# Optimization experiments

Measured on AMD Instinct MI355X. Metric: run time of the kernel, lower is better.

Reference implementation:

```python
import jax, jax.numpy as jnp
import numpy as np
import math

G = 8; N0 = 16384; DEG = 8; E = G * N0 * DEG
C = 128; H = 256; OUT = 128; L = 3
RATIO = 0.5; EPS_FA = 0.1


def setup_inputs():
    key = jax.random.key(0)
    ks = jax.random.split(key, 10)
    x = jax.random.normal(ks[0], (G * N0, C), jnp.float32)
    e = jax.random.randint(ks[1], (2, E), 0, N0)
    off = jnp.repeat(jnp.arange(G) * N0, N0 * DEG)  # per-graph node offsets
    edge_index = (e + off[None, :]).astype(jnp.int32)  # (2, E), edges stay within their graph
    batch = jnp.repeat(jnp.arange(G), N0).astype(jnp.int32)
    root = jax.random.normal(ks[2], (G, C), jnp.float32)
    s = 0.05
    att_l = jax.random.normal(ks[3], (L, C), jnp.float32) * s
    att_r = jax.random.normal(ks[4], (L, C), jnp.float32) * s
    w_ih = jax.random.normal(ks[5], (3 * H, C * L), jnp.float32) * s
    w_hh = jax.random.normal(ks[6], (3 * H, H), jnp.float32) * s
    b_ih = jnp.zeros(3 * H, jnp.float32)
    b_hh = jnp.zeros(3 * H, jnp.float32)
    w_fin = jax.random.normal(ks[7], (OUT, H), jnp.float32) * s
    b_fin = jnp.zeros(OUT, jnp.float32)
    w_root = jax.random.normal(ks[8], (OUT, C), jnp.float32) * s
    b_root = jnp.zeros(OUT, jnp.float32)
    residual_alpha = jnp.float32(0.5)
    return dict(x=x, edge_index=edge_index, batch=batch, root=root, att_l=att_l, att_r=att_r,
                w_ih=w_ih, w_hh=w_hh, b_ih=b_ih, b_hh=b_hh, w_fin=w_fin, b_fin=b_fin,
                w_root=w_root, b_root=b_root, residual_alpha=residual_alpha)


def _faconv(xc, x0, src, dst, emask, al_w, ar_w, n):
    # gcn_norm with self-loops: deg over dst (+1 for self loop), w_ij = d_i^-1/2 d_j^-1/2
    deg = jax.ops.segment_sum(emask, dst, num_segments=n) + 1.0
    dinv = jax.lax.rsqrt(deg)
    w = dinv[src] * dinv[dst] * emask
    al = xc @ al_w  # (n,)
    ar = xc @ ar_w
    alpha = jnp.tanh(al[dst] + ar[src])
    out = jax.ops.segment_sum((w * alpha)[:, None] * xc[src], dst, num_segments=n)
    # self-loop message (weight 1/deg_i, alpha = tanh(al_i + ar_i))
    out = out + ((dinv * dinv) * jnp.tanh(al + ar))[:, None] * xc
    return out + EPS_FA * x0


def _forward(x, root, att_l, att_r, w_ih, w_hh, b_ih, b_hh, w_fin, b_fin, w_root, b_root, residual_alpha, edge_index):
    src = edge_index[0]
    dst = edge_index[1]
    emask = jnp.ones(src.shape[0], jnp.float32)  # edge validity mask (replaces dynamic edge filtering)
    cur, orig = x, x
    npg = N0  # nodes per graph at current layer (static)
    outs = []
    for i in range(L):
        n = G * npg
        h = jax.nn.relu(_faconv(cur, orig, src, dst, emask, att_l[i], att_r[i], n))
        outs.append(h.reshape(G, npg, C).max(axis=1))  # global_max_pool per graph
        # ASTGPool: score = out-degree on edge_index[0], per-graph top-k (k = ceil(npg*ratio))
        score = jax.ops.segment_sum(emask, src, num_segments=n)
        k = int(math.ceil(npg * RATIO))
        _, idx = jax.lax.top_k(score.reshape(G, npg), k)
        perm = (idx + (jnp.arange(G) * npg)[:, None]).reshape(-1)  # (G*k,) global kept-node ids
        keep = jnp.zeros(n, bool).at[perm].set(True)
        emask = emask * keep[src].astype(jnp.float32) * keep[dst].astype(jnp.float32)
        nmap = jnp.zeros(n, src.dtype).at[perm].set(jnp.arange(G * k, dtype=src.dtype))
        src, dst = nmap[src], nmap[dst]  # dead edges map to node 0 but have emask==0
        cur, orig, npg = h[perm], orig[perm], k  # multiplier = 1.0
    fused = jnp.concatenate(outs, axis=1)  # (G, C*L)
    # single-step GRU with h0 = 0
    gi = fused @ w_ih.T + b_ih
    ir, iz, inn = jnp.split(gi, 3, axis=1)
    br, bz, bn = jnp.split(b_hh, 3)
    r = jax.nn.sigmoid(ir + br)
    z = jax.nn.sigmoid(iz + bz)
    ncand = jnp.tanh(inn + r * bn)
    hgru = (1.0 - z) * ncand
    gnn_emb = hgru @ w_fin.T + b_fin
    root_emb = root @ w_root.T + b_root
    return residual_alpha * gnn_emb + (1.0 - residual_alpha) * root_emb


def reference(x, edge_index, batch, root, att_l, att_r, w_ih, w_hh, b_ih, b_hh, w_fin, b_fin, w_root, b_root, residual_alpha):
    del batch  # graphs are contiguous equal-size blocks; batch structure is encoded in G, N0
    return _forward(x, root, att_l, att_r, w_ih, w_hh, b_ih, b_hh, w_fin, b_fin, w_root, b_root, residual_alpha, edge_index)
```

## Files before the change

kernel.cpp:

```cpp
#include <hip/hip_runtime.h>
#include <math.h>

#define G 8
#define N0 16384
#define NEDGE (G*N0*8)
#define EPG (NEDGE/G)
#define C 128
#define EPS_FA 0.1f
#define SMAX 2048

typedef unsigned short ushort_t;
typedef unsigned int uint_t;

__device__ inline ushort_t f2bf(float f) {
    uint_t u = __float_as_uint(f);
    uint_t r = (u + 0x7FFFu + ((u >> 16) & 1u)) >> 16;
    return (ushort_t)r;
}
__device__ inline uint_t pack2bf(float a, float b) {
    return (uint_t)f2bf(a) | ((uint_t)f2bf(b) << 16);
}
__device__ inline float bflo(uint_t w) { return __uint_as_float(w << 16); }
__device__ inline float bfhi(uint_t w) { return __uint_as_float(w & 0xFFFF0000u); }

__global__ void __launch_bounds__(256) k_hist0(const int* __restrict__ ei,
                                               unsigned int* __restrict__ bh,
                                               ushort_t* __restrict__ lrank) {
    __shared__ unsigned int h[N0];
    int t = threadIdx.x;
    for (int i = t; i < N0; i += 256) h[i] = 0;
    __syncthreads();
    int base = blockIdx.x * 8192;
    int gbase = (blockIdx.x >> 4) * N0;
    for (int i = t; i < 8192; i += 256) {
        int s = ei[base + i] - gbase;
        int d = ei[NEDGE + base + i] - gbase;
        unsigned int old = atomicAdd(&h[d], 1u);
        lrank[base + i] = (ushort_t)(old & 0xFFFFu);
        atomicAdd(&h[s], 0x10000u);
    }
    __syncthreads();
    unsigned int* o = bh + (size_t)blockIdx.x * N0;
    for (int i = t; i < N0; i += 256) o[i] = h[i];
}

__global__ void __launch_bounds__(256) k_sumdeg_alar(
        unsigned int* __restrict__ bh, int* __restrict__ degI, int* __restrict__ score,
        float* __restrict__ pooled,
        const float* __restrict__ x, const float* __restrict__ attl,
        const float* __restrict__ attr, float* __restrict__ al, float* __restrict__ ar,
        ushort_t* __restrict__ xb) {
    int t = threadIdx.x;
    if ((int)blockIdx.x < 512) {
        int i = blockIdx.x * 256 + t;
        if (i < G * 384) pooled[i] = 0.0f;
        unsigned int* p = bh + ((size_t)((i >> 14) * 16) << 14) + (i & 16383);
        unsigned int run = 0; int as = 0;
        for (int b = 0; b < 16; b++) {
            unsigned int w = p[(size_t)b << 14];
            p[(size_t)b << 14] = run;
            run += w & 0xFFFFu; as += (int)(w >> 16);
        }
        degI[i] = (int)run; score[i] = as;
    } else {
        int idx = (blockIdx.x - 512) * 256 + t;
        int wid = idx >> 6, lane = idx & 63;
        float2 v  = ((const float2*)(x + (size_t)wid * C))[lane];
        ((uint_t*)(xb + (size_t)wid * C))[lane] = pack2bf(v.x, v.y);
        float2 l2 = ((const float2*)attl)[lane];
        float2 r2 = ((const float2*)attr)[lane];
        float sl = v.x * l2.x + v.y * l2.y;
        float sr = v.x * r2.x + v.y * r2.y;
        for (int o = 32; o >= 1; o >>= 1) { sl += __shfl_xor(sl, o); sr += __shfl_xor(sr, o); }
        if (lane == 0) { al[wid] = sl; ar[wid] = sr; }
    }
}

__global__ void k_sumdeg(unsigned int* __restrict__ bh, int* __restrict__ degI,
                         int* __restrict__ score, int shift, int nsub, int n) {
    int i = blockIdx.x * 256 + threadIdx.x;
    if (i >= n) return;
    int bins = 1 << shift;
    int g = i >> shift, u = i & (bins - 1);
    unsigned int* p = bh + ((size_t)(g * nsub) << shift) + u;
    unsigned int run = 0; int as = 0;
    for (int b = 0; b < nsub; b++) {
        unsigned int w = p[(size_t)b * bins];
        p[(size_t)b * bins] = run;
        run += w & 0xFFFFu; as += (int)(w >> 16);
    }
    degI[i] = (int)run; score[i] = as;
}

__global__ void __launch_bounds__(256) k_scan1(const int* __restrict__ degI,
                                               int* __restrict__ rowptr,
                                               int* __restrict__ bsum) {
    __shared__ int part[256];
    int t = threadIdx.x;
    int base = blockIdx.x * 2048 + t * 8;
    int v[8]; int s = 0;
    for (int i = 0; i < 8; i++) { v[i] = degI[base + i]; s += v[i]; }
    part[t] = s; __syncthreads();
    for (int o = 1; o < 256; o <<= 1) {
        int val = part[t];
        int add = (t >= o) ? part[t - o] : 0;
        __syncthreads();
        part[t] = val + add;
        __syncthreads();
    }
    int run = (t == 0) ? 0 : part[t - 1];
    if (t == 255) bsum[blockIdx.x] = part[255];
    for (int i = 0; i < 8; i++) { rowptr[base + i] = run; run += v[i]; }
}

__global__ void k_scan3s(int* __restrict__ rowptr,
                         const int* __restrict__ bsum, const int* __restrict__ degI,
                         const float* __restrict__ al, const float* __restrict__ ar,
                         float* __restrict__ dinv, float* __restrict__ selfco,
                         unsigned char* __restrict__ keep, int* __restrict__ nmap, int n) {
    __shared__ int base_s;
    int t = threadIdx.x;
    if (t < 64) {
        int c = blockIdx.x >> 3;
        int vv = (t < c) ? bsum[t] : 0;
        for (int o = 32; o >= 1; o >>= 1) vv += __shfl_xor(vv, o);
        if (t == 0) base_s = vv;
    }
    __syncthreads();
    int i = blockIdx.x * 256 + t;
    if (i >= n) return;
    rowptr[i] += base_s;
    float d  = (float)degI[i] + 1.0f;
    float di = rsqrtf(d);
    dinv[i]   = di;
    selfco[i] = di * di * tanhf(al[i] + ar[i]);
    keep[i] = 0; nmap[i] = 0;
}

__global__ void __launch_bounds__(256) k_fill_hist(
        const int* __restrict__ src, const int* __restrict__ dst,
        const unsigned char* __restrict__ em,
        const float* __restrict__ dinv, const float* __restrict__ al,
        const float* __restrict__ ar,
        const int* __restrict__ rowptr, const unsigned int* __restrict__ bpre,
        const ushort_t* __restrict__ lrank, int2* __restrict__ edges,
        int ebShift, int nsubShift, int binShift,
        const int* __restrict__ score, int npg, int nb,
        int* __restrict__ blockhist, int histBlocks) {
    __shared__ int lh[SMAX];
    int t = threadIdx.x;
    if ((int)blockIdx.x < histBlocks) {
        int g = blockIdx.x / nb, b = blockIdx.x % nb;
        for (int s = t; s < SMAX; s += 256) lh[s] = 0;
        __syncthreads();
        int s = score[g * npg + b * 256 + t];
        if (s > SMAX - 1) s = SMAX - 1;
        atomicAdd(&lh[s], 1);
        __syncthreads();
        int* outp = blockhist + ((size_t)g * nb + b) * SMAX;
        for (int i = t; i < SMAX; i += 256) outp[i] = lh[i];
    } else {
        int fb = blockIdx.x - histBlocks;
        int gph = fb & 7, chunk = fb >> 3;
        int e = gph * EPG + chunk * 256 + t;
        if (em && !em[e]) return;
        int s = src[e], d = dst[e];
        float cf = dinv[s] * dinv[d] * tanhf(al[d] + ar[s]);
        int b = e >> ebShift;
        int gb = (b >> nsubShift) << binShift;
        int slot = rowptr[d] + (int)bpre[((size_t)b << binShift) + (d - gb)] + (int)lrank[e];
        edges[slot] = make_int2(s, __float_as_int(cf));
    }
}

#define ACC4(W, CF) { a0 += (CF) * bflo((W).x); a1 += (CF) * bfhi((W).x); \
                      a2 += (CF) * bflo((W).y); a3 += (CF) * bfhi((W).y); }
__global__ void __launch_bounds__(256) k_msg_bp(
        const int* __restrict__ rowptr, const int* __restrict__ degI,
        const int2* __restrict__ edges,
        const ushort_t* __restrict__ cur, const ushort_t* __restrict__ xb,
        const int* __restrict__ oidx, const float* __restrict__ selfco,
        ushort_t* __restrict__ h, float* __restrict__ pb, int npg,
        int* __restrict__ blockhist, int* __restrict__ histT, int nb, int bpBlocks) {
    __shared__ float pm[8 * 128];
    __shared__ int tile[4096];
    int t = threadIdx.x;
    if ((int)blockIdx.x < bpBlocks) {
        int g = blockIdx.x >> 5, ch = blockIdx.x & 31;
        int s0 = ch * 64;
        int* bg = blockhist + (size_t)g * nb * SMAX;
        int tot = nb * 64;
        for (int i = t; i < tot; i += 256)
            tile[i] = bg[(size_t)(i >> 6) * SMAX + s0 + (i & 63)];
        __syncthreads();
        if (t < 64) {
            int acc = 0;
            for (int b = 0; b < nb; b++) {
                int idx = b * 64 + t;
                int v = tile[idx]; tile[idx] = acc; acc += v;
            }
            histT[g * SMAX + s0 + t] = acc;
        }
        __syncthreads();
        for (int i = t; i < tot; i += 256)
            bg[(size_t)(i >> 6) * SMAX + s0 + (i & 63)] = tile[i];
        return;
    }
    int mb   = blockIdx.x - bpBlocks;
    int g    = mb & 7;
    int ib   = mb >> 3;
    int sub  = t >> 5;
    int lane = t & 31;
    int v = g * npg + ib * 8 + sub;
    int rs = rowptr[v], deg = degI[v];
    int o = oidx ? oidx[v] : v;
    uint2 cw = ((const uint2*)(cur + (size_t)v * C))[lane];
    uint2 xw = ((const uint2*)(xb  + (size_t)o * C))[lane];
    float sc = selfco[v];
    float a0 = 0.0f, a1 = 0.0f, a2 = 0.0f, a3 = 0.0f;
    for (int j0 = 0; j0 < deg; j0 += 32) {
        int cnt = deg - j0; if (cnt > 32) cnt = 32;
        int2 er = make_int2(0, 0);
        if (lane < cnt) er = edges[rs + j0 + lane];
        uint2 w0 = make_uint2(0,0), w1 = w0, w2 = w0, w3 = w0;
        {
            int s0 = __shfl(er.x, 0, 32);
            if (0 < cnt) w0 = ((const uint2*)(cur + (size_t)s0 * C))[lane];
            int s1 = __shfl(er.x, 1, 32);
            if (1 < cnt) w1 = ((const uint2*)(cur + (size_t)s1 * C))[lane];
            int s2 = __shfl(er.x, 2, 32);
            if (2 < cnt) w2 = ((const uint2*)(cur + (size_t)s2 * C))[lane];
            int s3 = __shfl(er.x, 3, 32);
            if (3 < cnt) w3 = ((const uint2*)(cur + (size_t)s3 * C))[lane];
        }
        int j = 0;
        for (; j + 4 <= cnt; j += 4) {
            float cf0 = __int_as_float(__shfl(er.y, j, 32));
            ACC4(w0, cf0);
            int sn0 = __shfl(er.x, j + 4, 32);
            if (j + 4 < cnt) w0 = ((const uint2*)(cur + (size_t)sn0 * C))[lane];
            float cf1 = __int_as_float(__shfl(er.y, j + 1, 32));
            ACC4(w1, cf1);
            int sn1 = __shfl(er.x, j + 5, 32);
            if (j + 5 < cnt) w1 = ((const uint2*)(cur + (size_t)sn1 * C))[lane];
            float cf2 = __int_as_float(__shfl(er.y, j + 2, 32));
            ACC4(w2, cf2);
            int sn2 = __shfl(er.x, j + 6, 32);
            if (j + 6 < cnt) w2 = ((const uint2*)(cur + (size_t)sn2 * C))[lane];
            float cf3 = __int_as_float(__shfl(er.y, j + 3, 32));
            ACC4(w3, cf3);
            int sn3 = __shfl(er.x, j + 7, 32);
            if (j + 7 < cnt) w3 = ((const uint2*)(cur + (size_t)sn3 * C))[lane];
        }
        if (j < cnt)     { float cf = __int_as_float(__shfl(er.y, j,     32)); ACC4(w0, cf); }
        if (j + 1 < cnt) { float cf = __int_as_float(__shfl(er.y, j + 1, 32)); ACC4(w1, cf); }
        if (j + 2 < cnt) { float cf = __int_as_float(__shfl(er.y, j + 2, 32)); ACC4(w2, cf); }
    }
    float r0 = fmaxf(a0 + sc * bflo(cw.x) + EPS_FA * bflo(xw.x), 0.0f);
    float r1 = fmaxf(a1 + sc * bfhi(cw.x) + EPS_FA * bfhi(xw.x), 0.0f);
    float r2 = fmaxf(a2 + sc * bflo(cw.y) + EPS_FA * bflo(xw.y), 0.0f);
    float r3 = fmaxf(a3 + sc * bfhi(cw.y) + EPS_FA * bfhi(xw.y), 0.0f);
    uint2 hw; hw.x = pack2bf(r0, r1); hw.y = pack2bf(r2, r3);
    ((uint2*)(h + (size_t)v * C))[lane] = hw;
    float4 rr = make_float4(r0, r1, r2, r3);
    ((float4*)(pm + sub * 128))[lane] = rr;
    __syncthreads();
    if (t < 128) {
        float m = pm[t];
        for (int s = 1; s < 8; s++) m = fmaxf(m, pm[s * 128 + t]);
        pb[(size_t)mb * 128 + t] = m;
    }
}

__global__ void __launch_bounds__(256) k_pool_rank(
        const float* __restrict__ pb, float* __restrict__ pooled, int layer,
        const int* __restrict__ score, const int* __restrict__ blockhist,
        const int* __restrict__ hist, int npg, int nb, int k,
        unsigned char* __restrict__ keep, int* __restrict__ nmap,
        int* __restrict__ perm, int rankBlocks) {
    __shared__ int bp[SMAX];
    __shared__ int part[256];
    __shared__ int cs[256];
    __shared__ float sm[256];
    int t = threadIdx.x;
    if ((int)blockIdx.x < rankBlocks) {
        int g = blockIdx.x / nb, b = blockIdx.x % nb;
        const int* hg = hist + g * SMAX;
        int v[8]; int smv = 0;
        for (int i = 0; i < 8; i++) { v[i] = hg[SMAX - 1 - (t * 8 + i)]; smv += v[i]; }
        part[t] = smv; __syncthreads();
        for (int o = 1; o < 256; o <<= 1) {
            int val = part[t];
            int add = (t >= o) ? part[t - o] : 0;
            __syncthreads();
            part[t] = val + add;
            __syncthreads();
        }
        int run = (t == 0) ? 0 : part[t - 1];
        for (int i = 0; i < 8; i++) { bp[SMAX - 1 - (t * 8 + i)] = run; run += v[i]; }
        int vv = b * 256 + t;
        int s = score[g * npg + vv];
        if (s > SMAX - 1) s = SMAX - 1;
        cs[t] = s;
        __syncthreads();
        int cnt = 0;
        for (int u = 0; u < t; u++) cnt += (cs[u] == s);
        int pos = bp[s] + blockhist[((size_t)g * nb + b) * SMAX + s] + cnt;
        if (pos < k) {
            int vg = g * npg + vv;
            int nid = g * k + pos;
            keep[vg] = 1; nmap[vg] = nid; perm[nid] = vg;
        }
    } else {
        int pr = blockIdx.x - rankBlocks;
        int g = pr & 7, ch = pr >> 3;
        int c = t & 127, half = t >> 7;
        float m = 0.0f;
        for (int i = 0; i < 32; i++) {
            int r = ch * 64 + half * 32 + i;
            m = fmaxf(m, pb[(size_t)(g + 8 * r) * 128 + c]);
        }
        sm[t] = m;
        __syncthreads();
        if (t < 128) {
            float mm = fmaxf(sm[t], sm[t + 128]);
            atomicMax((unsigned int*)&pooled[g * 384 + layer * 128 + c], __float_as_uint(mm));
        }
    }
}

__global__ void __launch_bounds__(256) k_gather_remap(
        const ushort_t* __restrict__ h, const int* __restrict__ perm,
        const int* __restrict__ oidx,
        const float* __restrict__ attlN, const float* __restrict__ attrN,
        ushort_t* __restrict__ curN, int* __restrict__ oidxN,
        float* __restrict__ al, float* __restrict__ ar, int m,
        const int* __restrict__ inS, const int* __restrict__ inD,
        const unsigned char* __restrict__ inEm,
        int* __restrict__ src, int* __restrict__ dst, unsigned char* __restrict__ em,
        const unsigned char* __restrict__ keep, const int* __restrict__ nmap,
        unsigned int* __restrict__ bh, ushort_t* __restrict__ lrank, int kN) {
    __shared__ unsigned int hh[8192];
    int t = threadIdx.x;
    if ((int)blockIdx.x < 256) {
        for (int i = t; i < kN; i += 256) hh[i] = 0;
        __syncthreads();
        int base = blockIdx.x * 4096;
        int gb = (blockIdx.x >> 5) * kN;
        for (int i = t; i < 4096; i += 256) {
            int e = base + i;
            int s = inS[e], d = inD[e];
            bool ok = (!inEm || inEm[e]) && keep[s] && keep[d];
            if (ok) {
                int ns = nmap[s], nd = nmap[d];
                src[e] = ns; dst[e] = nd; em[e] = 1;
                unsigned int old = atomicAdd(&hh[nd - gb], 1u);
                lrank[e] = (ushort_t)(old & 0xFFFFu);
                atomicAdd(&hh[ns - gb], 0x10000u);
            } else { src[e] = 0; dst[e] = 0; em[e] = 0; }
        }
        __syncthreads();
        unsigned int* o = bh + (size_t)blockIdx.x * kN;
        for (int i = t; i < kN; i += 256) o[i] = hh[i];
    } else {
        int i = (blockIdx.x - 256) * 256 + t;
        int j = i >> 5, c4 = i & 31;
        int p = perm[j];
        uint2 w = ((const uint2*)(h + (size_t)p * C))[c4];
        ((uint2*)(curN + (size_t)j * C))[c4] = w;
        float f0 = bflo(w.x), f1 = bfhi(w.x), f2 = bflo(w.y), f3 = bfhi(w.y);
        float4 l4 = ((const float4*)attlN)[c4];
        float4 r4 = ((const float4*)attrN)[c4];
        float sl = f0 * l4.x + f1 * l4.y + f2 * l4.z + f3 * l4.w;
        float sr = f0 * r4.x + f1 * r4.y + f2 * r4.z + f3 * r4.w;
        for (int o = 16; o >= 1; o >>= 1) { sl += __shfl_xor(sl, o); sr += __shfl_xor(sr, o); }
        if (c4 == 0) {
            al[j] = sl; ar[j] = sr;
            oidxN[j] = oidx ? oidx[p] : p;
        }
    }
}

__global__ void __launch_bounds__(256) k_gi(const float* __restrict__ pooled,
                                            const float* __restrict__ wih,
                                            const float* __restrict__ bih,
                                            float* __restrict__ gi) {
    int g = blockIdx.y;
    int row = blockIdx.x * 4 + (threadIdx.x >> 6);
    int lane = threadIdx.x & 63;
    const float* w = wih + (size_t)row * 384;
    const float* f = pooled + g * 384;
    float s = 0.0f;
    #pragma unroll
    for (int i = 0; i < 6; i++) s += w[i * 64 + lane] * f[i * 64 + lane];
    for (int o = 32; o >= 1; o >>= 1) s += __shfl_xor(s, o);
    if (lane == 0) gi[g * 768 + row] = s + bih[row];
}

__global__ void __launch_bounds__(256) k_gru_fin(const float* __restrict__ gi,
        const float* __restrict__ bhh, const float* __restrict__ wfin,
        const float* __restrict__ bfin, const float* __restrict__ wroot,
        const float* __restrict__ broot, const float* __restrict__ rootv,
        const float* __restrict__ alphap, float* __restrict__ out) {
    int g = blockIdx.x, t = threadIdx.x;
    __shared__ float hg[256];
    {
        float r  = 1.0f / (1.0f + expf(-(gi[g * 768 + t]       + bhh[t])));
        float z  = 1.0f / (1.0f + expf(-(gi[g * 768 + 256 + t] + bhh[256 + t])));
        float nc = tanhf(gi[g * 768 + 512 + t] + r * bhh[512 + t]);
        hg[t] = (1.0f - z) * nc;
    }
    __syncthreads();
    float a = alphap[0];
    int wv = t >> 6, lane = t & 63;
    const float* rg = rootv + (size_t)g * 128;
    for (int oo = 0; oo < 32; oo++) {
        int o = wv * 32 + oo;
        const float* wf = wfin + (size_t)o * 256;
        float sf = wf[lane] * hg[lane] + wf[64 + lane] * hg[64 + lane]
                 + wf[128 + lane] * hg[128 + lane] + wf[192 + lane] * hg[192 + lane];
        const float* wr = wroot + (size_t)o * 128;
        float sr = wr[lane] * rg[lane] + wr[64 + lane] * rg[64 + lane];
        float s = a * sf + (1.0f - a) * sr;
        for (int sh = 32; sh >= 1; sh >>= 1) s += __shfl_xor(s, sh);
        if (lane == 0)
            out[g * 128 + o] = s + a * bfin[o] + (1.0f - a) * broot[o];
    }
}

extern "C" void kernel_launch(void* const* d_in, const int* in_sizes, int n_in,
                              void* d_out, int out_size, void* d_ws, size_t ws_size,
                              hipStream_t stream) {
    const float* x      = (const float*)d_in[0];
    const int*   ei     = (const int*)d_in[1];
    const float* rootv  = (const float*)d_in[3];
    const float* att_l  = (const float*)d_in[4];
    const float* att_r  = (const float*)d_in[5];
    const float* w_ih   = (const float*)d_in[6];
    const float* b_ih   = (const float*)d_in[8];
    const float* b_hh   = (const float*)d_in[9];
    const float* w_fin  = (const float*)d_in[10];
    const float* b_fin  = (const float*)d_in[11];
    const float* w_root = (const float*)d_in[12];
    const float* b_root = (const float*)d_in[13];
    const float* alphap = (const float*)d_in[14];
    float* out = (float*)d_out;

    char* wsb = (char*)d_ws;
    size_t off = 0;
    auto alloc = [&](size_t bytes) -> char* {
        char* p = wsb + off; off += (bytes + 255) & ~(size_t)255; return p;
    };
    ushort_t* xb   = (ushort_t*)alloc((size_t)131072 * C * 2);
    ushort_t* bufH = (ushort_t*)alloc((size_t)131072 * C * 2);
    ushort_t* bufC = (ushort_t*)alloc((size_t)65536  * C * 2);
    int*   srcA   = (int*)alloc((size_t)NEDGE * 4);
    int*   dstA   = (int*)alloc((size_t)NEDGE * 4);
    unsigned char* emask = (unsigned char*)alloc(NEDGE);
    int2*  edges  = (int2*)alloc((size_t)NEDGE * 8);
    ushort_t* lrank = (ushort_t*)alloc((size_t)NEDGE * 2);
    float* al     = (float*)alloc(131072 * 4);
    float* ar     = (float*)alloc(131072 * 4);
    float* dinv   = (float*)alloc(131072 * 4);
    float* selfco = (float*)alloc(131072 * 4);
    int*   degI   = (int*)alloc(131072 * 4);
    int*   score  = (int*)alloc(131072 * 4);
    int*   rowptr = (int*)alloc(131072 * 4);
    int*   bsum   = (int*)alloc(256 * 4);
    unsigned char* keep = (unsigned char*)alloc(131072);
    int*   nmap   = (int*)alloc(131072 * 4);
    int*   perm   = (int*)alloc(65536 * 4);
    int*   oidxA  = (int*)alloc(65536 * 4);
    int*   oidxB  = (int*)alloc(32768 * 4);
    float* pooled = (float*)alloc(G * 384 * 4);
    float* giBuf  = (float*)alloc(G * 768 * 4);
    int*   blockhist = (int*)alloc((size_t)G * 64 * SMAX * 4);
    int*   histT  = (int*)alloc((size_t)G * SMAX * 4);
    unsigned int* bh = (unsigned int*)alloc((size_t)128 * N0 * 4);
    float* pb = (float*)bh;

    k_hist0<<<128, 256, 0, stream>>>(ei, bh, lrank);
    k_sumdeg_alar<<<512 + 32768, 256, 0, stream>>>(bh, degI, score, pooled,
                                                   x, att_l, att_r, al, ar, xb);

    const int ns[3]   = {131072, 65536, 32768};
    const int npgs[3] = {16384, 8192, 4096};
    const int ks[3]   = {8192, 4096, 0};
    const int shifts[3] = {14, 13, 12};

    for (int l = 0; l < 3; l++) {
        int n = ns[l], npg = npgs[l], k = ks[l];
        const ushort_t* cur = (l == 0) ? xb : bufC;
        const int* oidx = (l == 0) ? nullptr : (l == 1 ? oidxA : oidxB);
        int* oidxN = (l == 0) ? oidxA : oidxB;
        const int* eS = (l == 0) ? ei : srcA;
        const int* eD = (l == 0) ? ei + NEDGE : dstA;
        const unsigned char* eM = (l == 0) ? nullptr : emask;
        int ebShift   = (l == 0) ? 13 : 12;
        int nsubShift = (l == 0) ? 4  : 5;
        int binShift  = shifts[l];
        int nb = npg / 256;

        k_scan1<<<n / 2048, 256, 0, stream>>>(degI, rowptr, bsum);
        k_scan3s<<<n / 256, 256, 0, stream>>>(rowptr, bsum, degI, al, ar,
                                              dinv, selfco, keep, nmap, n);

        int histBlocks = (l < 2) ? G * nb : 0;
        k_fill_hist<<<histBlocks + NEDGE / 256, 256, 0, stream>>>(
            eS, eD, eM, dinv, al, ar, rowptr, bh, lrank, edges,
            ebShift, nsubShift, binShift, score, npg, nb, blockhist, histBlocks);

        int bpBlocks = (l < 2) ? 256 : 0;
        k_msg_bp<<<bpBlocks + n / 8, 256, 0, stream>>>(
            rowptr, degI, edges, cur, xb, oidx, selfco, bufH, pb, npg,
            blockhist, histT, nb, bpBlocks);

        int rankBlocks = (l < 2) ? G * nb : 0;
        k_pool_rank<<<rankBlocks + npg / 64, 256, 0, stream>>>(
            pb, pooled, l, score, blockhist, histT, npg, nb, k,
            keep, nmap, perm, rankBlocks);

        if (l < 2) {
            int m = G * k;
            k_gather_remap<<<256 + m / 8, 256, 0, stream>>>(
                bufH, perm, oidx, att_l + (l + 1) * C, att_r + (l + 1) * C,
                bufC, oidxN, al, ar, m,
                eS, eD, eM, srcA, dstA, emask, keep, nmap, bh, lrank, k);
            k_sumdeg<<<(G * k + 255) / 256, 256, 0, stream>>>(bh, degI, score,
                                                              shifts[l + 1], 32, G * k);
        }
    }

    k_gi<<<dim3(192, G), 256, 0, stream>>>(pooled, w_ih, b_ih, giBuf);
    k_gru_fin<<<G, 256, 0, stream>>>(giBuf, b_hh, w_fin, b_fin, w_root, b_root,
                                     rootv, alphap, out);
}
```

Before: 402.8 us.

## Fuse degree sum and prefix scan into single decoupled-lookback scan kernel

Merges the per-bin degree summation, the two-pass block scan and the dinv/selfco computation into one kernel that uses a decoupled lookback across blocks with flag-tagged state words. Per-node data is packed into float4/int4 records so the edge-fill and message kernels each do one vector load instead of several scattered loads. The message loop drops its per-edge bounds predicates by clamping indices to the last valid edge. This removes several kernel launches and intermediate buffers, but relies on inter-block spinning, which is only safe if earlier blocks are scheduled before later ones.

```diff
diff --git a/kernel.cpp b/kernel.cpp
--- a/kernel.cpp
+++ b/kernel.cpp
@@ -8,6 +8,8 @@
 #define C 128
 #define EPS_FA 0.1f
 #define SMAX 2048
+#define FLAGA (1u<<30)
+#define FLAGP (2u<<30)
 
 typedef unsigned short ushort_t;
 typedef unsigned int uint_t;
@@ -44,63 +46,49 @@
     for (int i = t; i < N0; i += 256) o[i] = h[i];
 }
 
-__global__ void __launch_bounds__(256) k_sumdeg_alar(
-        unsigned int* __restrict__ bh, int* __restrict__ degI, int* __restrict__ score,
-        float* __restrict__ pooled,
-        const float* __restrict__ x, const float* __restrict__ attl,
-        const float* __restrict__ attr, float* __restrict__ al, float* __restrict__ ar,
-        ushort_t* __restrict__ xb) {
-    int t = threadIdx.x;
-    if ((int)blockIdx.x < 512) {
-        int i = blockIdx.x * 256 + t;
-        if (i < G * 384) pooled[i] = 0.0f;
-        unsigned int* p = bh + ((size_t)((i >> 14) * 16) << 14) + (i & 16383);
-        unsigned int run = 0; int as = 0;
-        for (int b = 0; b < 16; b++) {
-            unsigned int w = p[(size_t)b << 14];
-            p[(size_t)b << 14] = run;
-            run += w & 0xFFFFu; as += (int)(w >> 16);
-        }
-        degI[i] = (int)run; score[i] = as;
-    } else {
-        int idx = (blockIdx.x - 512) * 256 + t;
-        int wid = idx >> 6, lane = idx & 63;
-        float2 v  = ((const float2*)(x + (size_t)wid * C))[lane];
-        ((uint_t*)(xb + (size_t)wid * C))[lane] = pack2bf(v.x, v.y);
-        float2 l2 = ((const float2*)attl)[lane];
-        float2 r2 = ((const float2*)attr)[lane];
-        float sl = v.x * l2.x + v.y * l2.y;
-        float sr = v.x * r2.x + v.y * r2.y;
-        for (int o = 32; o >= 1; o >>= 1) { sl += __shfl_xor(sl, o); sr += __shfl_xor(sr, o); }
-        if (lane == 0) { al[wid] = sl; ar[wid] = sr; }
-    }
-}
-
-__global__ void k_sumdeg(unsigned int* __restrict__ bh, int* __restrict__ degI,
-                         int* __restrict__ score, int shift, int nsub, int n) {
-    int i = blockIdx.x * 256 + threadIdx.x;
-    if (i >= n) return;
-    int bins = 1 << shift;
-    int g = i >> shift, u = i & (bins - 1);
-    unsigned int* p = bh + ((size_t)(g * nsub) << shift) + u;
+__global__ void __launch_bounds__(256) k_alar(const float* __restrict__ x,
+                       const float* __restrict__ attl, const float* __restrict__ attr,
+                       float* __restrict__ al, float* __restrict__ ar,
+                       ushort_t* __restrict__ xb, float* __restrict__ pooled,
+                       unsigned int* __restrict__ scanstate) {
+    int gidx = blockIdx.x * 256 + threadIdx.x;
+    if (gidx < 3072) pooled[gidx] = 0.0f;
+    if (gidx < 1536) scanstate[gidx] = 0u;
+    int wid = gidx >> 6, lane = gidx & 63;
+    float2 v  = ((const float2*)(x + (size_t)wid * C))[lane];
+    ((uint_t*)(xb + (size_t)wid * C))[lane] = pack2bf(v.x, v.y);
+    float2 l2 = ((const float2*)attl)[lane];
+    float2 r2 = ((const float2*)attr)[lane];
+    float sl = v.x * l2.x + v.y * l2.y;
+    float sr = v.x * r2.x + v.y * r2.y;
+    for (int o = 32; o >= 1; o >>= 1) { sl += __shfl_xor(sl, o); sr += __shfl_xor(sr, o); }
+    if (lane == 0) { al[wid] = sl; ar[wid] = sr; }
+}
+
+__global__ void __launch_bounds__(256) k_scan(
+        unsigned int* __restrict__ bh, int shiftBins, int nsub,
+        const float* __restrict__ al, const float* __restrict__ ar,
+        const int* __restrict__ oidx,
+        int* __restrict__ score, float4* __restrict__ fillinfo,
+        int4* __restrict__ nodeinfo,
+        unsigned char* __restrict__ keep, int* __restrict__ nmap,
+        unsigned int* __restrict__ state) {
+    __shared__ int part[256];
+    __shared__ int sbase;
+    int b = blockIdx.x, t = threadIdx.x;
+    int i = b * 256 + t;
+    int bins = 1 << shiftBins;
+    int g = i >> shiftBins, u = i & (bins - 1);
+    unsigned int* p = bh + ((size_t)(g * nsub) << shiftBins) + u;
     unsigned int run = 0; int as = 0;
-    for (int b = 0; b < nsub; b++) {
-        unsigned int w = p[(size_t)b * bins];
-        p[(size_t)b * bins] = run;
+    for (int bb = 0; bb < nsub; bb++) {
+        unsigned int w = p[(size_t)bb << shiftBins];
+        p[(size_t)bb << shiftBins] = run;
         run += w & 0xFFFFu; as += (int)(w >> 16);
     }
-    degI[i] = (int)run; score[i] = as;
-}
-
-__global__ void __launch_bounds__(256) k_scan1(const int* __restrict__ degI,
-                                               int* __restrict__ rowptr,
-                                               int* __restrict__ bsum) {
-    __shared__ int part[256];
-    int t = threadIdx.x;
-    int base = blockIdx.x * 2048 + t * 8;
-    int v[8]; int s = 0;
-    for (int i = 0; i < 8; i++) { v[i] = degI[base + i]; s += v[i]; }
-    part[t] = s; __syncthreads();
+    int deg = (int)run;
+    score[i] = as;
+    part[t] = deg; __syncthreads();
     for (int o = 1; o < 256; o <<= 1) {
         int val = part[t];
         int add = (t >= o) ? part[t - o] : 0;
@@ -108,41 +96,53 @@
         part[t] = val + add;
         __syncthreads();
     }
-    int run = (t == 0) ? 0 : part[t - 1];
-    if (t == 255) bsum[blockIdx.x] = part[255];
-    for (int i = 0; i < 8; i++) { rowptr[base + i] = run; run += v[i]; }
-}
-
-__global__ void k_scan3s(int* __restrict__ rowptr,
-                         const int* __restrict__ bsum, const int* __restrict__ degI,
-                         const float* __restrict__ al, const float* __restrict__ ar,
-                         float* __restrict__ dinv, float* __restrict__ selfco,
-                         unsigned char* __restrict__ keep, int* __restrict__ nmap, int n) {
-    __shared__ int base_s;
-    int t = threadIdx.x;
+    int incl = part[t];
+    int S = part[255];
     if (t < 64) {
-        int c = blockIdx.x >> 3;
-        int vv = (t < c) ? bsum[t] : 0;
-        for (int o = 32; o >= 1; o >>= 1) vv += __shfl_xor(vv, o);
-        if (t == 0) base_s = vv;
+        if (b == 0) {
+            if (t == 0) { sbase = 0; __threadfence(); atomicExch(&state[0], FLAGP | (unsigned)S); }
+        } else {
+            if (t == 0) { __threadfence(); atomicExch(&state[b], FLAGA | (unsigned)S); }
+            int base = 0;
+            int p0 = b - 1;
+            while (true) {
+                int idx = p0 - (int)t;
+                unsigned int st;
+                if (idx >= 0) {
+                    do { st = atomicAdd(&state[idx], 0u); } while ((st >> 30) == 0);
+                } else st = FLAGP;
+                unsigned long long pm = __ballot((st >> 30) == 2);
+                bool anyP = (pm != 0ull);
+                int firstP = anyP ? (int)(__ffsll((long long)pm) - 1) : 64;
+                int contrib = ((int)t <= firstP) ? (int)(st & 0x3FFFFFFFu) : 0;
+                for (int o2 = 32; o2 >= 1; o2 >>= 1) contrib += __shfl_xor(contrib, o2);
+                base += contrib;
+                if (anyP) break;
+                p0 -= 64;
+            }
+            if (t == 0) {
+                sbase = base;
+                __threadfence(); atomicExch(&state[b], FLAGP | (unsigned)(base + S));
+            }
+        }
     }
     __syncthreads();
-    int i = blockIdx.x * 256 + t;
-    if (i >= n) return;
-    rowptr[i] += base_s;
-    float d  = (float)degI[i] + 1.0f;
-    float di = rsqrtf(d);
-    dinv[i]   = di;
-    selfco[i] = di * di * tanhf(al[i] + ar[i]);
+    int rp = sbase + incl - deg;
+    float df = (float)deg + 1.0f;
+    float di = rsqrtf(df);
+    float a = al[i], r = ar[i];
+    float sc = di * di * tanhf(a + r);
+    int o = oidx ? oidx[i] : i;
+    fillinfo[i] = make_float4(di, a, r, __int_as_float(rp));
+    nodeinfo[i] = make_int4(rp, deg, __float_as_int(sc), o);
     keep[i] = 0; nmap[i] = 0;
 }
 
 __global__ void __launch_bounds__(256) k_fill_hist(
         const int* __restrict__ src, const int* __restrict__ dst,
         const unsigned char* __restrict__ em,
-        const float* __restrict__ dinv, const float* __restrict__ al,
-        const float* __restrict__ ar,
-        const int* __restrict__ rowptr, const unsigned int* __restrict__ bpre,
+        const float4* __restrict__ fillinfo,
+        const unsigned int* __restrict__ bpre,
         const ushort_t* __restrict__ lrank, int2* __restrict__ edges,
         int ebShift, int nsubShift, int binShift,
         const int* __restrict__ score, int npg, int nb,
@@ -165,10 +165,13 @@
         int e = gph * EPG + chunk * 256 + t;
         if (em && !em[e]) return;
         int s = src[e], d = dst[e];
-        float cf = dinv[s] * dinv[d] * tanhf(al[d] + ar[s]);
+        float4 fs = fillinfo[s];
+        float4 fd = fillinfo[d];
+        float cf = fs.x * fd.x * tanhf(fd.y + fs.z);
         int b = e >> ebShift;
         int gb = (b >> nsubShift) << binShift;
-        int slot = rowptr[d] + (int)bpre[((size_t)b << binShift) + (d - gb)] + (int)lrank[e];
+        int slot = __float_as_int(fd.w)
+                 + (int)bpre[((size_t)b << binShift) + (d - gb)] + (int)lrank[e];
         edges[slot] = make_int2(s, __float_as_int(cf));
     }
 }
@@ -176,10 +179,9 @@
 #define ACC4(W, CF) { a0 += (CF) * bflo((W).x); a1 += (CF) * bfhi((W).x); \
                       a2 += (CF) * bflo((W).y); a3 += (CF) * bfhi((W).y); }
 __global__ void __launch_bounds__(256) k_msg_bp(
-        const int* __restrict__ rowptr, const int* __restrict__ degI,
+        const int4* __restrict__ nodeinfo,
         const int2* __restrict__ edges,
         const ushort_t* __restrict__ cur, const ushort_t* __restrict__ xb,
-        const int* __restrict__ oidx, const float* __restrict__ selfco,
         ushort_t* __restrict__ h, float* __restrict__ pb, int npg,
         int* __restrict__ blockhist, int* __restrict__ histT, int nb, int bpBlocks) {
     __shared__ float pm[8 * 128];
@@ -212,45 +214,46 @@
     int sub  = t >> 5;
     int lane = t & 31;
     int v = g * npg + ib * 8 + sub;
-    int rs = rowptr[v], deg = degI[v];
-    int o = oidx ? oidx[v] : v;
+    int4 ni = nodeinfo[v];
+    int rs = ni.x, deg = ni.y;
+    float sc = __int_as_float(ni.z);
+    int o = ni.w;
     uint2 cw = ((const uint2*)(cur + (size_t)v * C))[lane];
     uint2 xw = ((const uint2*)(xb  + (size_t)o * C))[lane];
-    float sc = selfco[v];
     float a0 = 0.0f, a1 = 0.0f, a2 = 0.0f, a3 = 0.0f;
     for (int j0 = 0; j0 < deg; j0 += 32) {
         int cnt = deg - j0; if (cnt > 32) cnt = 32;
-        int2 er = make_int2(0, 0);
-        if (lane < cnt) er = edges[rs + j0 + lane];
-        uint2 w0 = make_uint2(0,0), w1 = w0, w2 = w0, w3 = w0;
+        int last = cnt - 1;
+        int2 er = edges[rs + j0 + (lane < last ? lane : last)];
+        uint2 w0, w1, w2, w3;
         {
             int s0 = __shfl(er.x, 0, 32);
-            if (0 < cnt) w0 = ((const uint2*)(cur + (size_t)s0 * C))[lane];
-            int s1 = __shfl(er.x, 1, 32);
-            if (1 < cnt) w1 = ((const uint2*)(cur + (size_t)s1 * C))[lane];
-            int s2 = __shfl(er.x, 2, 32);
-            if (2 < cnt) w2 = ((const uint2*)(cur + (size_t)s2 * C))[lane];
-            int s3 = __shfl(er.x, 3, 32);
-            if (3 < cnt) w3 = ((const uint2*)(cur + (size_t)s3 * C))[lane];
+            w0 = ((const uint2*)(cur + (size_t)s0 * C))[lane];
+            int s1 = __shfl(er.x, 1 < last ? 1 : last, 32);
+            w1 = ((const uint2*)(cur + (size_t)s1 * C))[lane];
+            int s2 = __shfl(er.x, 2 < last ? 2 : last, 32);
+            w2 = ((const uint2*)(cur + (size_t)s2 * C))[lane];
+            int s3 = __shfl(er.x, 3 < last ? 3 : last, 32);
+            w3 = ((const uint2*)(cur + (size_t)s3 * C))[lane];
         }
         int j = 0;
         for (; j + 4 <= cnt; j += 4) {
             float cf0 = __int_as_float(__shfl(er.y, j, 32));
             ACC4(w0, cf0);
-            int sn0 = __shfl(er.x, j + 4, 32);
-            if (j + 4 < cnt) w0 = ((const uint2*)(cur + (size_t)sn0 * C))[lane];
+            int sn0 = __shfl(er.x, (j + 4) < last ? (j + 4) : last, 32);
+            w0 = ((const uint2*)(cur + (size_t)sn0 * C))[lane];
             float cf1 = __int_as_float(__shfl(er.y, j + 1, 32));
             ACC4(w1, cf1);
-            int sn1 = __shfl(er.x, j + 5, 32);
-            if (j + 5 < cnt) w1 = ((const uint2*)(cur + (size_t)sn1 * C))[lane];
+            int sn1 = __shfl(er.x, (j + 5) < last ? (j + 5) : last, 32);
+            w1 = ((const uint2*)(cur + (size_t)sn1 * C))[lane];
             float cf2 = __int_as_float(__shfl(er.y, j + 2, 32));
             ACC4(w2, cf2);
-            int sn2 = __shfl(er.x, j + 6, 32);
-            if (j + 6 < cnt) w2 = ((const uint2*)(cur + (size_t)sn2 * C))[lane];
+            int sn2 = __shfl(er.x, (j + 6) < last ? (j + 6) : last, 32);
+            w2 = ((const uint2*)(cur + (size_t)sn2 * C))[lane];
             float cf3 = __int_as_float(__shfl(er.y, j + 3, 32));
             ACC4(w3, cf3);
-            int sn3 = __shfl(er.x, j + 7, 32);
-            if (j + 7 < cnt) w3 = ((const uint2*)(cur + (size_t)sn3 * C))[lane];
+            int sn3 = __shfl(er.x, (j + 7) < last ? (j + 7) : last, 32);
+            w3 = ((const uint2*)(cur + (size_t)sn3 * C))[lane];
         }
         if (j < cnt)     { float cf = __int_as_float(__shfl(er.y, j,     32)); ACC4(w0, cf); }
         if (j + 1 < cnt) { float cf = __int_as_float(__shfl(er.y, j + 1, 32)); ACC4(w1, cf); }
@@ -461,12 +464,9 @@
     ushort_t* lrank = (ushort_t*)alloc((size_t)NEDGE * 2);
     float* al     = (float*)alloc(131072 * 4);
     float* ar     = (float*)alloc(131072 * 4);
-    float* dinv   = (float*)alloc(131072 * 4);
-    float* selfco = (float*)alloc(131072 * 4);
-    int*   degI   = (int*)alloc(131072 * 4);
     int*   score  = (int*)alloc(131072 * 4);
-    int*   rowptr = (int*)alloc(131072 * 4);
-    int*   bsum   = (int*)alloc(256 * 4);
+    float4* fillinfo = (float4*)alloc((size_t)131072 * 16);
+    int4*   nodeinfo = (int4*)alloc((size_t)131072 * 16);
     unsigned char* keep = (unsigned char*)alloc(131072);
     int*   nmap   = (int*)alloc(131072 * 4);
     int*   perm   = (int*)alloc(65536 * 4);
@@ -474,19 +474,20 @@
     int*   oidxB  = (int*)alloc(32768 * 4);
     float* pooled = (float*)alloc(G * 384 * 4);
     float* giBuf  = (float*)alloc(G * 768 * 4);
+    unsigned int* scanstate = (unsigned int*)alloc(1536 * 4);
     int*   blockhist = (int*)alloc((size_t)G * 64 * SMAX * 4);
     int*   histT  = (int*)alloc((size_t)G * SMAX * 4);
     unsigned int* bh = (unsigned int*)alloc((size_t)128 * N0 * 4);
     float* pb = (float*)bh;
 
     k_hist0<<<128, 256, 0, stream>>>(ei, bh, lrank);
-    k_sumdeg_alar<<<512 + 32768, 256, 0, stream>>>(bh, degI, score, pooled,
-                                                   x, att_l, att_r, al, ar, xb);
+    k_alar<<<32768, 256, 0, stream>>>(x, att_l, att_r, al, ar, xb, pooled, scanstate);
 
     const int ns[3]   = {131072, 65536, 32768};
     const int npgs[3] = {16384, 8192, 4096};
     const int ks[3]   = {8192, 4096, 0};
     const int shifts[3] = {14, 13, 12};
+    const int stoff[3]  = {0, 512, 768};
 
     for (int l = 0; l < 3; l++) {
         int n = ns[l], npg = npgs[l], k = ks[l];
@@ -498,21 +499,22 @@
         const unsigned char* eM = (l == 0) ? nullptr : emask;
         int ebShift   = (l == 0) ? 13 : 12;
         int nsubShift = (l == 0) ? 4  : 5;
+        int nsub      = (l == 0) ? 16 : 32;
         int binShift  = shifts[l];
         int nb = npg / 256;
 
-        k_scan1<<<n / 2048, 256, 0, stream>>>(degI, rowptr, bsum);
-        k_scan3s<<<n / 256, 256, 0, stream>>>(rowptr, bsum, degI, al, ar,
-                                              dinv, selfco, keep, nmap, n);
+        k_scan<<<n / 256, 256, 0, stream>>>(bh, binShift, nsub, al, ar, oidx,
+                                            score, fillinfo, nodeinfo, keep, nmap,
+                                            scanstate + stoff[l]);
 
         int histBlocks = (l < 2) ? G * nb : 0;
         k_fill_hist<<<histBlocks + NEDGE / 256, 256, 0, stream>>>(
-            eS, eD, eM, dinv, al, ar, rowptr, bh, lrank, edges,
+            eS, eD, eM, fillinfo, bh, lrank, edges,
             ebShift, nsubShift, binShift, score, npg, nb, blockhist, histBlocks);
 
         int bpBlocks = (l < 2) ? 256 : 0;
         k_msg_bp<<<bpBlocks + n / 8, 256, 0, stream>>>(
-            rowptr, degI, edges, cur, xb, oidx, selfco, bufH, pb, npg,
+            nodeinfo, edges, cur, xb, bufH, pb, npg,
             blockhist, histT, nb, bpBlocks);
 
         int rankBlocks = (l < 2) ? G * nb : 0;
@@ -526,8 +528,6 @@
                 bufH, perm, oidx, att_l + (l + 1) * C, att_r + (l + 1) * C,
                 bufC, oidxN, al, ar, m,
                 eS, eD, eM, srcA, dstA, emask, keep, nmap, bh, lrank, k);
-            k_sumdeg<<<(G * k + 255) / 256, 256, 0, stream>>>(bh, degI, score,
-                                                              shifts[l + 1], 32, G * k);
         }
     }
 
```

New measurement: 443.0 us. +10.0%, slower.
